# Kernel optimization log

Hardware: AMD Instinct MI355X
Metric: run time of the kernel (lower is better)

The kernel has to match this reference:

```python
import jax, jax.numpy as jnp
import numpy as np
from jax import lax

VOCAB = 50257
BEAM = 8
BSZ = 64
STEP = 16
NGRAM = 4
CAND_MULT = 2


def setup_inputs() -> dict:
    key = jax.random.key(0)
    k1, k2, k3 = jax.random.split(key, 3)
    lprobs = jax.random.normal(k1, (BSZ, BEAM, VOCAB), dtype=jnp.float32)
    scores = jax.random.normal(k2, (BSZ, BEAM, STEP), dtype=jnp.float32)
    mask = jax.random.randint(k3, (BSZ, BEAM, NGRAM), 0, 2, dtype=jnp.int32)
    return {"lprobs": lprobs, "scores": scores, "mask": mask, "step": STEP}


def reference(lprobs, scores, mask, step):
    bsz, beam_size, vocab_size = lprobs.shape
    k = CAND_MULT * beam_size

    # mask: (b, beam, n_gram) -> keep beam only if all n_gram entries nonzero
    # (original repeats over vocab then sums; summing first is equivalent and
    # avoids materializing the (b, beam, vocab, n_gram) tensor)
    n_gram = mask.shape[-1]
    keep = jnp.sum(mask, axis=-1) == n_gram  # (b, beam) bool
    lprobs = jnp.where(keep[:, :, None], lprobs, 0.0)

    if step == 0:
        lprobs = lprobs[:, 0:1, :]
        beam_size = 1
    else:
        # broadcast-add previous cumulative score of each beam
        lprobs = lprobs + scores[:, :, step - 1][:, :, None]

    flat = lprobs.reshape(bsz, beam_size * vocab_size)
    scores_buf, indices_flat = lax.top_k(flat, k)  # (b, k)
    beams_buf = indices_flat // vocab_size
    indices_buf = indices_flat % vocab_size
    return scores_buf, indices_buf, beams_buf
```

## Files before the change

kernel.cpp:

```cpp
#include <hip/hip_runtime.h>

#define VOCAB 50257
#define BEAM  8
#define BSZ   64
#define KSEL  16
#define CHUNK 4
#define TPB   256
#define PER   12568
#define NCAND (BEAM * CHUNK * KSEL)
#define CAP   1024

__device__ __forceinline__ unsigned int ord32(float f) {
    unsigned int u = __float_as_uint(f);
    return (u & 0x80000000u) ? ~u : (u | 0x80000000u);
}
__device__ __forceinline__ float unord32(unsigned int o) {
    unsigned int u = (o & 0x80000000u) ? (o & 0x7FFFFFFFu) : ~o;
    return __uint_as_float(u);
}

__device__ __forceinline__ unsigned long long mkkey(float v, unsigned int flat) {
    return ((unsigned long long)ord32(v) << 32) | (0xFFFFFFFFu - flat);
}

__global__ __launch_bounds__(TPB)
void beam_topk_scan(const float* __restrict__ lprobs,
                    const float* __restrict__ scores,
                    const int*   __restrict__ mask,
                    const int*   __restrict__ stepp,
                    unsigned long long* __restrict__ ws)
{
    const int blk   = blockIdx.x;
    const int chunk = blk % CHUNK;
    const int beam  = (blk / CHUNK) % BEAM;
    const int b     = blk / (CHUNK * BEAM);
    const int tid   = threadIdx.x;
    const int step  = stepp[0];

    unsigned long long* okeys = ws + (size_t)blk * KSEL;

    const int  bb   = b * BEAM + beam;
    const int* m    = mask + bb * 4;
    const bool keep = (m[0] + m[1] + m[2] + m[3]) == 4;
    const float sadd  = (step == 0) ? 0.0f : scores[bb * 16 + (step - 1)];
    const bool active = (step != 0) || (beam == 0);

    if (!active || (!keep && chunk != 0)) {
        if (tid < KSEL) okeys[tid] = 0ull;
        return;
    }
    if (!keep) {
        if (tid < KSEL)
            okeys[tid] = mkkey(sadd, (unsigned)(beam * VOCAB + tid));
        return;
    }

    __shared__ unsigned long long tmax[TPB];
    __shared__ unsigned long long cand[CAP];
    __shared__ unsigned long long theta_s;
    __shared__ int ccount;

    const int lo  = chunk * PER;
    const int len = ((lo + PER < VOCAB) ? PER : (VOCAB - lo));
    const float* base = lprobs + (size_t)bb * VOCAB;
    const float4* base4 = (const float4*)(base + lo);
    const unsigned int fb = (unsigned)(beam * VOCAB + lo);
    const int nv4 = (len + 3) >> 2;

    unsigned long long m0 = 0ull, m1 = 0ull, m2 = 0ull, m3 = 0ull;
    int j = tid;
    for (; j + 3 * TPB < nv4 - 1 || (j + 3 * TPB == nv4 - 1 && (len & 3) == 0); j += 4 * TPB) {
        const float4 v0 = base4[j];
        const float4 v1 = base4[j + TPB];
        const float4 v2 = base4[j + 2 * TPB];
        const float4 v3 = base4[j + 3 * TPB];
        unsigned long long k;
        const unsigned e0 = fb + 4u * (unsigned)j;
        const unsigned e1 = fb + 4u * (unsigned)(j + TPB);
        const unsigned e2 = fb + 4u * (unsigned)(j + 2 * TPB);
        const unsigned e3 = fb + 4u * (unsigned)(j + 3 * TPB);
        k = mkkey(v0.x + sadd, e0);     if (k > m0) m0 = k;
        k = mkkey(v0.y + sadd, e0 + 1); if (k > m0) m0 = k;
        k = mkkey(v0.z + sadd, e0 + 2); if (k > m0) m0 = k;
        k = mkkey(v0.w + sadd, e0 + 3); if (k > m0) m0 = k;
        k = mkkey(v1.x + sadd, e1);     if (k > m1) m1 = k;
        k = mkkey(v1.y + sadd, e1 + 1); if (k > m1) m1 = k;
        k = mkkey(v1.z + sadd, e1 + 2); if (k > m1) m1 = k;
        k = mkkey(v1.w + sadd, e1 + 3); if (k > m1) m1 = k;
        k = mkkey(v2.x + sadd, e2);     if (k > m2) m2 = k;
        k = mkkey(v2.y + sadd, e2 + 1); if (k > m2) m2 = k;
        k = mkkey(v2.z + sadd, e2 + 2); if (k > m2) m2 = k;
        k = mkkey(v2.w + sadd, e2 + 3); if (k > m2) m2 = k;
        k = mkkey(v3.x + sadd, e3);     if (k > m3) m3 = k;
        k = mkkey(v3.y + sadd, e3 + 1); if (k > m3) m3 = k;
        k = mkkey(v3.z + sadd, e3 + 2); if (k > m3) m3 = k;
        k = mkkey(v3.w + sadd, e3 + 3); if (k > m3) m3 = k;
    }
    for (; j < nv4; j += TPB) {
        const int e = 4 * j;
        #pragma unroll
        for (int u = 0; u < 4; ++u) {
            if (e + u < len) {
                const unsigned long long k = mkkey(base[lo + e + u] + sadd,
                                                   fb + (unsigned)(e + u));
                if (k > m0) m0 = k;
            }
        }
    }
    if (m1 > m0) m0 = m1;
    if (m2 > m0) m0 = m2;
    if (m3 > m0) m0 = m3;
    const unsigned long long mx = m0;

    tmax[tid] = mx;
    if (tid == 0) ccount = 0;
    __syncthreads();

    int r = 0;
    for (int jj = 0; jj < TPB; ++jj) r += (tmax[jj] > mx) ? 1 : 0;
    if (r == KSEL - 1) theta_s = mx;
    __syncthreads();
    const unsigned long long theta = theta_s;

    if (mx >= theta) {
        for (int jj = tid; jj < nv4; jj += TPB) {
            const int e = 4 * jj;
            if (e + 3 < len) {
                const float4 v = base4[jj];
                const unsigned eb = fb + (unsigned)e;
                unsigned long long k;
                k = mkkey(v.x + sadd, eb);     if (k >= theta) cand[atomicAdd(&ccount,1)] = k;
                k = mkkey(v.y + sadd, eb + 1); if (k >= theta) cand[atomicAdd(&ccount,1)] = k;
                k = mkkey(v.z + sadd, eb + 2); if (k >= theta) cand[atomicAdd(&ccount,1)] = k;
                k = mkkey(v.w + sadd, eb + 3); if (k >= theta) cand[atomicAdd(&ccount,1)] = k;
            } else {
                #pragma unroll
                for (int u = 0; u < 4; ++u) {
                    if (e + u < len) {
                        const unsigned long long k =
                            mkkey(base[lo + e + u] + sadd, fb + (unsigned)(e + u));
                        if (k >= theta) cand[atomicAdd(&ccount,1)] = k;
                    }
                }
            }
        }
    }
    __syncthreads();
    const int n = ccount;

    for (int c = tid; c < n; c += TPB) {
        const unsigned long long k0 = cand[c];
        int rank = 0;
        for (int jj = 0; jj < n; ++jj) rank += (cand[jj] > k0) ? 1 : 0;
        if (rank < KSEL) okeys[rank] = k0;
    }
}

__global__ __launch_bounds__(TPB)
void beam_topk_select(const unsigned long long* __restrict__ ws,
                      float* __restrict__ out)
{
    const int b   = blockIdx.x;
    const int tid = threadIdx.x;
    __shared__ unsigned long long keys[NCAND];
    const unsigned long long* src = ws + (size_t)b * NCAND;
    for (int i = tid; i < NCAND; i += TPB) keys[i] = src[i];
    __syncthreads();

    for (int c = tid; c < NCAND; c += TPB) {
        const unsigned long long k0 = keys[c];
        if (k0 == 0ull) continue;
        int rank = 0;
        for (int j = 0; j < NCAND; ++j) rank += (keys[j] > k0) ? 1 : 0;
        if (rank < KSEL) {
            const unsigned int flat = 0xFFFFFFFFu - (unsigned)(k0 & 0xFFFFFFFFull);
            const float val = unord32((unsigned)(k0 >> 32));
            const int vi = (int)(flat % VOCAB);
            const int bi = (int)(flat / VOCAB);
            out[b * KSEL + rank]                   = val;
            out[BSZ * KSEL + b * KSEL + rank]      = (float)vi;
            out[2 * BSZ * KSEL + b * KSEL + rank]  = (float)bi;
        }
    }
}

extern "C" void kernel_launch(void* const* d_in, const int* in_sizes, int n_in,
                              void* d_out, int out_size, void* d_ws, size_t ws_size,
                              hipStream_t stream)
{
    const float* lprobs = (const float*)d_in[0];
    const float* scores = (const float*)d_in[1];
    const int*   mask   = (const int*)d_in[2];
    const int*   stepp  = (const int*)d_in[3];
    float* out = (float*)d_out;
    unsigned long long* ws = (unsigned long long*)d_ws;

    hipLaunchKernelGGL(beam_topk_scan, dim3(BSZ * BEAM * CHUNK), dim3(TPB), 0, stream,
                       lprobs, scores, mask, stepp, ws);
    hipLaunchKernelGGL(beam_topk_select, dim3(BSZ), dim3(TPB), 0, stream, ws, out);
}
```

Measured before the change: 156.6 us.

## Fuse scan and select kernels with spin-wait finisher and parallelize candidate rescan

Merges the per-chunk scan and per-row select into one kernel: designated finisher blocks poll workspace slots with atomic loads until all producer blocks of the row have published their top-16 keys, then do the final ranking. A memset initializes the workspace so unpublished slots are detectable. The candidate rescan is redistributed so all threads share the strided loads of the 16 winning threads instead of only those threads scanning serially. This risks spin-waiting cost and relies on forward progress of producer blocks.

```diff
diff --git a/kernel.cpp b/kernel.cpp
--- a/kernel.cpp
+++ b/kernel.cpp
@@ -7,28 +7,41 @@
 #define CHUNK 4
 #define TPB   256
 #define PER   12568
-#define NCAND (BEAM * CHUNK * KSEL)
+#define BLKS_PER_ROW (BEAM * CHUNK)
+#define NCAND (BLKS_PER_ROW * KSEL)
 #define CAP   1024
-
-__device__ __forceinline__ unsigned int ord32(float f) {
+#define SLOTS 13
+#define EMPTY_KEY 1ull
+
+static __device__ __forceinline__ unsigned int ord32(float f) {
     unsigned int u = __float_as_uint(f);
     return (u & 0x80000000u) ? ~u : (u | 0x80000000u);
 }
-__device__ __forceinline__ float unord32(unsigned int o) {
+static __device__ __forceinline__ float unord32(unsigned int o) {
     unsigned int u = (o & 0x80000000u) ? (o & 0x7FFFFFFFu) : ~o;
     return __uint_as_float(u);
 }
-
-__device__ __forceinline__ unsigned long long mkkey(float v, unsigned int flat) {
+static __device__ __forceinline__ unsigned long long mkkey(float v, unsigned int flat) {
     return ((unsigned long long)ord32(v) << 32) | (0xFFFFFFFFu - flat);
 }
+static __device__ __forceinline__ void publish(unsigned long long* p, unsigned long long k) {
+    __hip_atomic_store(p, k, __ATOMIC_RELAXED, __HIP_MEMORY_SCOPE_AGENT);
+}
+static __device__ __forceinline__ unsigned long long poll(const unsigned long long* p) {
+    return __hip_atomic_load(p, __ATOMIC_RELAXED, __HIP_MEMORY_SCOPE_AGENT);
+}
+static __device__ __forceinline__ bool slot_valid(unsigned long long k) {
+    const unsigned int lo = (unsigned int)k;
+    return (lo == 1u) || (lo >= 0xFFF00000u);
+}
 
 __global__ __launch_bounds__(TPB)
-void beam_topk_scan(const float* __restrict__ lprobs,
-                    const float* __restrict__ scores,
-                    const int*   __restrict__ mask,
-                    const int*   __restrict__ stepp,
-                    unsigned long long* __restrict__ ws)
+void beam_topk_fused(const float* __restrict__ lprobs,
+                     const float* __restrict__ scores,
+                     const int*   __restrict__ mask,
+                     const int*   __restrict__ stepp,
+                     unsigned long long* __restrict__ ws,
+                     float* __restrict__ out)
 {
     const int blk   = blockIdx.x;
     const int chunk = blk % CHUNK;
@@ -37,113 +50,151 @@
     const int tid   = threadIdx.x;
     const int step  = stepp[0];
 
+    __shared__ unsigned long long tmax[TPB];
+    __shared__ unsigned long long cand[CAP];
+    __shared__ unsigned long long rowkeys[NCAND];
+    __shared__ unsigned long long theta_s;
+    __shared__ int ccount;
+    __shared__ int wcnt;
+    __shared__ int wid[KSEL];
+
     unsigned long long* okeys = ws + (size_t)blk * KSEL;
-
     const int  bb   = b * BEAM + beam;
     const int* m    = mask + bb * 4;
     const bool keep = (m[0] + m[1] + m[2] + m[3]) == 4;
     const float sadd  = (step == 0) ? 0.0f : scores[bb * 16 + (step - 1)];
     const bool active = (step != 0) || (beam == 0);
+    const bool finisher = (beam == 0) && (chunk == 0);
 
     if (!active || (!keep && chunk != 0)) {
-        if (tid < KSEL) okeys[tid] = 0ull;
-        return;
-    }
-    if (!keep) {
+        if (tid < KSEL) publish(&okeys[tid], EMPTY_KEY);
+    } else if (!keep) {
         if (tid < KSEL)
-            okeys[tid] = mkkey(sadd, (unsigned)(beam * VOCAB + tid));
-        return;
-    }
-
-    __shared__ unsigned long long tmax[TPB];
-    __shared__ unsigned long long cand[CAP];
-    __shared__ unsigned long long theta_s;
-    __shared__ int ccount;
-
-    const int lo  = chunk * PER;
-    const int len = ((lo + PER < VOCAB) ? PER : (VOCAB - lo));
-    const float* base = lprobs + (size_t)bb * VOCAB;
-    const float4* base4 = (const float4*)(base + lo);
-    const unsigned int fb = (unsigned)(beam * VOCAB + lo);
-    const int nv4 = (len + 3) >> 2;
-
-    unsigned long long m0 = 0ull, m1 = 0ull, m2 = 0ull, m3 = 0ull;
-    int j = tid;
-    for (; j + 3 * TPB < nv4 - 1 || (j + 3 * TPB == nv4 - 1 && (len & 3) == 0); j += 4 * TPB) {
-        const float4 v0 = base4[j];
-        const float4 v1 = base4[j + TPB];
-        const float4 v2 = base4[j + 2 * TPB];
-        const float4 v3 = base4[j + 3 * TPB];
-        unsigned long long k;
-        const unsigned e0 = fb + 4u * (unsigned)j;
-        const unsigned e1 = fb + 4u * (unsigned)(j + TPB);
-        const unsigned e2 = fb + 4u * (unsigned)(j + 2 * TPB);
-        const unsigned e3 = fb + 4u * (unsigned)(j + 3 * TPB);
-        k = mkkey(v0.x + sadd, e0);     if (k > m0) m0 = k;
-        k = mkkey(v0.y + sadd, e0 + 1); if (k > m0) m0 = k;
-        k = mkkey(v0.z + sadd, e0 + 2); if (k > m0) m0 = k;
-        k = mkkey(v0.w + sadd, e0 + 3); if (k > m0) m0 = k;
-        k = mkkey(v1.x + sadd, e1);     if (k > m1) m1 = k;
-        k = mkkey(v1.y + sadd, e1 + 1); if (k > m1) m1 = k;
-        k = mkkey(v1.z + sadd, e1 + 2); if (k > m1) m1 = k;
-        k = mkkey(v1.w + sadd, e1 + 3); if (k > m1) m1 = k;
-        k = mkkey(v2.x + sadd, e2);     if (k > m2) m2 = k;
-        k = mkkey(v2.y + sadd, e2 + 1); if (k > m2) m2 = k;
-        k = mkkey(v2.z + sadd, e2 + 2); if (k > m2) m2 = k;
-        k = mkkey(v2.w + sadd, e2 + 3); if (k > m2) m2 = k;
-        k = mkkey(v3.x + sadd, e3);     if (k > m3) m3 = k;
-        k = mkkey(v3.y + sadd, e3 + 1); if (k > m3) m3 = k;
-        k = mkkey(v3.z + sadd, e3 + 2); if (k > m3) m3 = k;
-        k = mkkey(v3.w + sadd, e3 + 3); if (k > m3) m3 = k;
-    }
-    for (; j < nv4; j += TPB) {
-        const int e = 4 * j;
-        #pragma unroll
-        for (int u = 0; u < 4; ++u) {
-            if (e + u < len) {
-                const unsigned long long k = mkkey(base[lo + e + u] + sadd,
-                                                   fb + (unsigned)(e + u));
-                if (k > m0) m0 = k;
+            publish(&okeys[tid], mkkey(sadd, (unsigned)(beam * VOCAB + tid)));
+    } else {
+        const int lo  = chunk * PER;
+        const int len = ((lo + PER < VOCAB) ? PER : (VOCAB - lo));
+        const float* base = lprobs + (size_t)bb * VOCAB;
+        const float4* base4 = (const float4*)(base + lo);
+        const unsigned int fb = (unsigned)(beam * VOCAB + lo);
+        const int nv4 = (len + 3) >> 2;
+
+        unsigned long long m0 = 0ull, m1 = 0ull, m2 = 0ull, m3 = 0ull;
+        int j = tid;
+        for (; j + 3 * TPB < nv4 - 1 || (j + 3 * TPB == nv4 - 1 && (len & 3) == 0);
+             j += 4 * TPB) {
+            const float4 v0 = base4[j];
+            const float4 v1 = base4[j + TPB];
+            const float4 v2 = base4[j + 2 * TPB];
+            const float4 v3 = base4[j + 3 * TPB];
+            unsigned long long k;
+            const unsigned e0 = fb + 4u * (unsigned)j;
+            const unsigned e1 = fb + 4u * (unsigned)(j + TPB);
+            const unsigned e2 = fb + 4u * (unsigned)(j + 2 * TPB);
+            const unsigned e3 = fb + 4u * (unsigned)(j + 3 * TPB);
+            k = mkkey(v0.x + sadd, e0);     if (k > m0) m0 = k;
+            k = mkkey(v0.y + sadd, e0 + 1); if (k > m0) m0 = k;
+            k = mkkey(v0.z + sadd, e0 + 2); if (k > m0) m0 = k;
+            k = mkkey(v0.w + sadd, e0 + 3); if (k > m0) m0 = k;
+            k = mkkey(v1.x + sadd, e1);     if (k > m1) m1 = k;
+            k = mkkey(v1.y + sadd, e1 + 1); if (k > m1) m1 = k;
+            k = mkkey(v1.z + sadd, e1 + 2); if (k > m1) m1 = k;
+            k = mkkey(v1.w + sadd, e1 + 3); if (k > m1) m1 = k;
+            k = mkkey(v2.x + sadd, e2);     if (k > m2) m2 = k;
+            k = mkkey(v2.y + sadd, e2 + 1); if (k > m2) m2 = k;
+            k = mkkey(v2.z + sadd, e2 + 2); if (k > m2) m2 = k;
+            k = mkkey(v2.w + sadd, e2 + 3); if (k > m2) m2 = k;
+            k = mkkey(v3.x + sadd, e3);     if (k > m3) m3 = k;
+            k = mkkey(v3.y + sadd, e3 + 1); if (k > m3) m3 = k;
+            k = mkkey(v3.z + sadd, e3 + 2); if (k > m3) m3 = k;
+            k = mkkey(v3.w + sadd, e3 + 3); if (k > m3) m3 = k;
+        }
+        for (; j < nv4; j += TPB) {
+            const int e = 4 * j;
+            #pragma unroll
+            for (int u = 0; u < 4; ++u) {
+                if (e + u < len) {
+                    const unsigned long long k = mkkey(base[lo + e + u] + sadd,
+                                                       fb + (unsigned)(e + u));
+                    if (k > m0) m0 = k;
+                }
             }
         }
-    }
-    if (m1 > m0) m0 = m1;
-    if (m2 > m0) m0 = m2;
-    if (m3 > m0) m0 = m3;
-    const unsigned long long mx = m0;
-
-    tmax[tid] = mx;
-    if (tid == 0) ccount = 0;
-    __syncthreads();
-
-    int r = 0;
-    for (int jj = 0; jj < TPB; ++jj) r += (tmax[jj] > mx) ? 1 : 0;
-    if (r == KSEL - 1) theta_s = mx;
-    __syncthreads();
-    const unsigned long long theta = theta_s;
-
-    if (mx >= theta) {
-        for (int jj = tid; jj < nv4; jj += TPB) {
-            const int e = 4 * jj;
-            if (e + 3 < len) {
-                const float4 v = base4[jj];
-                const unsigned eb = fb + (unsigned)e;
-                unsigned long long k;
-                k = mkkey(v.x + sadd, eb);     if (k >= theta) cand[atomicAdd(&ccount,1)] = k;
-                k = mkkey(v.y + sadd, eb + 1); if (k >= theta) cand[atomicAdd(&ccount,1)] = k;
-                k = mkkey(v.z + sadd, eb + 2); if (k >= theta) cand[atomicAdd(&ccount,1)] = k;
-                k = mkkey(v.w + sadd, eb + 3); if (k >= theta) cand[atomicAdd(&ccount,1)] = k;
-            } else {
-                #pragma unroll
-                for (int u = 0; u < 4; ++u) {
-                    if (e + u < len) {
-                        const unsigned long long k =
-                            mkkey(base[lo + e + u] + sadd, fb + (unsigned)(e + u));
-                        if (k >= theta) cand[atomicAdd(&ccount,1)] = k;
+        if (m1 > m0) m0 = m1;
+        if (m2 > m0) m0 = m2;
+        if (m3 > m0) m0 = m3;
+        const unsigned long long mx = m0;
+
+        tmax[tid] = mx;
+        if (tid == 0) { ccount = 0; wcnt = 0; }
+        __syncthreads();
+
+        int r = 0;
+        for (int jj = 0; jj < TPB; ++jj) r += (tmax[jj] > mx) ? 1 : 0;
+        if (r == KSEL - 1) theta_s = mx;
+        if (mx != 0ull) {  }
+        if (r < KSEL) {  }
+        __syncthreads();
+        const unsigned long long theta = theta_s;
+
+        if (mx >= theta) wid[atomicAdd(&wcnt, 1)] = tid;
+        __syncthreads();
+
+        for (int t = tid; t < KSEL * SLOTS; t += TPB) {
+            const int w  = wid[t / SLOTS];
+            const int jj = w + (t % SLOTS) * TPB;
+            if (jj < nv4) {
+                const int e = 4 * jj;
+                if (e + 3 < len) {
+                    const float4 v = base4[jj];
+                    const unsigned eb = fb + (unsigned)e;
+                    unsigned long long k;
+                    k = mkkey(v.x + sadd, eb);     if (k >= theta) cand[atomicAdd(&ccount,1)] = k;
+                    k = mkkey(v.y + sadd, eb + 1); if (k >= theta) cand[atomicAdd(&ccount,1)] = k;
+                    k = mkkey(v.z + sadd, eb + 2); if (k >= theta) cand[atomicAdd(&ccount,1)] = k;
+                    k = mkkey(v.w + sadd, eb + 3); if (k >= theta) cand[atomicAdd(&ccount,1)] = k;
+                } else {
+                    #pragma unroll
+                    for (int u = 0; u < 4; ++u) {
+                        if (e + u < len) {
+                            const unsigned long long k =
+                                mkkey(base[lo + e + u] + sadd, fb + (unsigned)(e + u));
+                            if (k >= theta) cand[atomicAdd(&ccount,1)] = k;
+                        }
                     }
                 }
             }
         }
+        __syncthreads();
+        const int n = ccount;
+
+        for (int c = tid; c < n; c += TPB) {
+            const unsigned long long k0 = cand[c];
+            int rank = 0;
+            for (int jj = 0; jj < n; ++jj) rank += (cand[jj] > k0) ? 1 : 0;
+            if (rank < KSEL) publish(&okeys[rank], k0);
+        }
+    }
+
+    if (!finisher) return;
+
+    const unsigned long long* src = ws + (size_t)b * NCAND;
+    for (int i = tid; i < NCAND; i += TPB) {
+        unsigned long long k;
+        for (;;) {
+            k = poll(&src[i]);
+            if (slot_valid(k)) break;
+            __builtin_amdgcn_s_sleep(2);
+        }
+        rowkeys[i] = k;
+    }
+    __syncthreads();
+    if (tid == 0) ccount = 0;
+    __syncthreads();
+
+    for (int i = tid; i < NCAND; i += TPB) {
+        const unsigned long long k = rowkeys[i];
+        if ((unsigned int)(k >> 32) != 0u) cand[atomicAdd(&ccount, 1)] = k;
     }
     __syncthreads();
     const int n = ccount;
@@ -152,34 +203,14 @@
         const unsigned long long k0 = cand[c];
         int rank = 0;
         for (int jj = 0; jj < n; ++jj) rank += (cand[jj] > k0) ? 1 : 0;
-        if (rank < KSEL) okeys[rank] = k0;
-    }
-}
-
-__global__ __launch_bounds__(TPB)
-void beam_topk_select(const unsigned long long* __restrict__ ws,
-                      float* __restrict__ out)
-{
-    const int b   = blockIdx.x;
-    const int tid = threadIdx.x;
-    __shared__ unsigned long long keys[NCAND];
-    const unsigned long long* src = ws + (size_t)b * NCAND;
-    for (int i = tid; i < NCAND; i += TPB) keys[i] = src[i];
-    __syncthreads();
-
-    for (int c = tid; c < NCAND; c += TPB) {
-        const unsigned long long k0 = keys[c];
-        if (k0 == 0ull) continue;
-        int rank = 0;
-        for (int j = 0; j < NCAND; ++j) rank += (keys[j] > k0) ? 1 : 0;
         if (rank < KSEL) {
-            const unsigned int flat = 0xFFFFFFFFu - (unsigned)(k0 & 0xFFFFFFFFull);
-            const float val = unord32((unsigned)(k0 >> 32));
+            const unsigned int flat = 0xFFFFFFFFu - (unsigned int)(k0 & 0xFFFFFFFFull);
+            const float val = unord32((unsigned int)(k0 >> 32));
             const int vi = (int)(flat % VOCAB);
             const int bi = (int)(flat / VOCAB);
-            out[b * KSEL + rank]                   = val;
-            out[BSZ * KSEL + b * KSEL + rank]      = (float)vi;
-            out[2 * BSZ * KSEL + b * KSEL + rank]  = (float)bi;
+            out[b * KSEL + rank]                  = val;
+            out[BSZ * KSEL + b * KSEL + rank]     = (float)vi;
+            out[2 * BSZ * KSEL + b * KSEL + rank] = (float)bi;
         }
     }
 }
@@ -195,7 +226,8 @@
     float* out = (float*)d_out;
     unsigned long long* ws = (unsigned long long*)d_ws;
 
-    hipLaunchKernelGGL(beam_topk_scan, dim3(BSZ * BEAM * CHUNK), dim3(TPB), 0, stream,
-                       lprobs, scores, mask, stepp, ws);
-    hipLaunchKernelGGL(beam_topk_select, dim3(BSZ), dim3(TPB), 0, stream, ws, out);
-}
+    hipMemsetAsync((void*)ws, 0, (size_t)BSZ * NCAND * sizeof(unsigned long long),
+                   stream);
+    hipLaunchKernelGGL(beam_topk_fused, dim3(BSZ * BEAM * CHUNK), dim3(TPB), 0, stream,
+                       lprobs, scores, mask, stepp, ws, out);
+}
```

After: 145.2 us. 1.08x faster.
